# Optimization experiments

Measured on AMD Instinct MI355X. Metric: run time of the kernel, lower is better.

## Reference

```python
import jax, jax.numpy as jnp
import numpy as np

UNITS = 32
BACKBONE = 64

def lecun_tanh(x):
    return 1.7159 * jnp.tanh(0.666 * x)

def setup_inputs() -> dict:
    key = jax.random.key(0)
    ks = jax.random.split(key, 6)
    B, C, T, H, W = 4, 16, 32, 64, 64
    scale_b = 1.0 / np.sqrt(C + UNITS)
    scale_h = 1.0 / np.sqrt(BACKBONE)
    return {
        "x": jax.random.normal(ks[0], (B, C, T, H, W), jnp.float32),
        "Wb": jax.random.normal(ks[1], (BACKBONE, C + UNITS), jnp.float32) * scale_b,
        "bb": jnp.zeros((BACKBONE,), jnp.float32),
        "Wff1": jax.random.normal(ks[2], (UNITS, BACKBONE), jnp.float32) * scale_h,
        "bff1": jnp.zeros((UNITS,), jnp.float32),
        "Wff2": jax.random.normal(ks[3], (UNITS, BACKBONE), jnp.float32) * scale_h,
        "bff2": jnp.zeros((UNITS,), jnp.float32),
        "Wta": jax.random.normal(ks[4], (UNITS, BACKBONE), jnp.float32) * scale_h,
        "bta": jnp.zeros((UNITS,), jnp.float32),
        "Wtb": jax.random.normal(ks[5], (UNITS, BACKBONE), jnp.float32) * scale_h,
        "btb": jnp.zeros((UNITS,), jnp.float32),
    }

def reference(x, Wb, bb, Wff1, bff1, Wff2, bff2, Wta, bta, Wtb, btb):
    # x: (B, C, T, H, W) -> time-major (T, B, C, H, W) for the scan
    xs = jnp.transpose(x, (2, 0, 1, 3, 4))
    B, C, H, W = x.shape[0], x.shape[1], x.shape[3], x.shape[4]
    h0 = jnp.zeros((B, UNITS, H, W), x.dtype)
    ts = jnp.asarray(1.0, x.dtype)  # no timespans provided -> ts = 1.0

    def head(z, Wh, bh):  # channel-wise (1x1) linear: (B,K,H,W) -> (B,U,H,W)
        return jnp.einsum('bkhw,uk->buhw', z, Wh) + bh[None, :, None, None]

    def step(h, xt):
        z = jnp.concatenate([xt, h], axis=1)  # (B, C+U, H, W)
        z = lecun_tanh(jnp.einsum('bchw,kc->bkhw', z, Wb) + bb[None, :, None, None])
        ff1 = jnp.tanh(head(z, Wff1, bff1))
        ff2 = jnp.tanh(head(z, Wff2, bff2))
        t_a = head(z, Wta, bta)
        t_b = head(z, Wtb, btb)
        t_interp = jax.nn.sigmoid(t_a * ts + t_b)
        h_new = ff1 * (1.0 - t_interp) + t_interp * ff2
        return h_new, h_new

    _, ys = jax.lax.scan(step, h0, xs)  # ys: (T, B, U, H, W)
    # stack along dim=1 (batch_first) then permute(0,2,1,3,4) -> (B, U, T, H, W)
    return jnp.transpose(ys, (1, 2, 0, 3, 4))
```

## Files before the change

kernel.cpp:

```cpp
#include <hip/hip_runtime.h>
#include <hip/hip_bf16.h>


#define CIN      16
#define UNITS    32
#define BACKBONE 64
#define CZ       48
#define TSTEPS   32
#define HW       4096
#define NPIX     16
#define NTHREADS 256

typedef __attribute__((ext_vector_type(8))) short  short8;
typedef __attribute__((ext_vector_type(8))) __bf16 bf16x8;
typedef __attribute__((ext_vector_type(4))) float  float4v;
typedef __attribute__((ext_vector_type(4))) unsigned int uint4v;

#define BAR_LDS() asm volatile("s_waitcnt lgkmcnt(0)\n\ts_barrier" ::: "memory")

__device__ __forceinline__ unsigned short bf16_rne(float f) {
    unsigned u = __float_as_uint(f);
    return (unsigned short)((u + 0x7FFFu + ((u >> 16) & 1u)) >> 16);
}
__device__ __forceinline__ float bf16_tof(unsigned short h) {
    return __uint_as_float(((unsigned)h) << 16);
}
__device__ __forceinline__ unsigned cvt_pk_bf16(float lo, float hi) {
    unsigned r;
    asm("v_cvt_pk_bf16_f32 %0, %1, %2" : "=v"(r) : "v"(lo), "v"(hi));
    return r;
}

#if __has_builtin(__builtin_amdgcn_exp2f)
#define EXP2F(x) __builtin_amdgcn_exp2f(x)
#else
#define EXP2F(x) __expf(0.69314718056f * (x))
#endif
#if __has_builtin(__builtin_amdgcn_rcpf)
#define RCPF(x) __builtin_amdgcn_rcpf(x)
#else
#define RCPF(x) __fdividef(1.0f, (x))
#endif

__device__ __forceinline__ float lecun_tanh_f(float v) {
    float e = EXP2F(1.92166925f * v);
    return fmaf(-3.4318f, RCPF(e + 1.0f), 1.7159f);
}
__device__ __forceinline__ float tanh_f(float v) {
    float e = EXP2F(2.88539008f * v);
    return fmaf(-2.0f, RCPF(e + 1.0f), 1.0f);
}
__device__ __forceinline__ float sigmoid_f(float v) {
    float e = EXP2F(-1.44269504f * v);
    return RCPF(1.0f + e);
}
__device__ __forceinline__ float4v mfma16(bf16x8 a, bf16x8 b, float4v c) {
    return __builtin_amdgcn_mfma_f32_16x16x32_bf16(a, b, c, 0, 0, 0);
}
__device__ __forceinline__ void split8(const float* v, bf16x8& hi, bf16x8& lo) {
    short8 sh, sl;
    #pragma unroll
    for (int j = 0; j < 8; ++j) {
        unsigned short h = bf16_rne(v[j]);
        sh[j] = (short)h;
        sl[j] = (short)bf16_rne(v[j] - bf16_tof(h));
    }
    hi = __builtin_bit_cast(bf16x8, sh);
    lo = __builtin_bit_cast(bf16x8, sl);
}

__global__ __launch_bounds__(NTHREADS, 4)
void cfc_mfma_kernel(const float* __restrict__ x,   const float* __restrict__ Wb,
                     const float* __restrict__ bb,
                     const float* __restrict__ Wff1, const float* __restrict__ bff1,
                     const float* __restrict__ Wff2, const float* __restrict__ bff2,
                     const float* __restrict__ Wta,  const float* __restrict__ bta,
                     const float* __restrict__ Wtb,  const float* __restrict__ btb,
                     float* __restrict__ out)
{
    __shared__ unsigned hbuf[4][64];
    __shared__ unsigned abuf[8][64];

    const int tid  = threadIdx.x;
    const int w    = tid >> 6;
    const int lane = tid & 63;
    const int ln   = lane & 15;
    const int lq   = lane >> 4;

    const int gpix = blockIdx.x * NPIX;
    const int b    = gpix >> 12;
    const int pinb = gpix & 4095;
    const int mt   = w;

    bf16x8 Whhi, Whlo;
    {
        float v[8];
        #pragma unroll
        for (int j = 0; j < 8; ++j)
            v[j] = Wb[(mt * 16 + ln) * CZ + CIN + lq * 8 + j];
        split8(v, Whhi, Whlo);
    }
    bf16x8 Wxhi, Wxlo;
    {
        float v[8];
        #pragma unroll
        for (int j = 0; j < 8; ++j)
            v[j] = (lq < 2) ? Wb[(mt * 16 + ln) * CZ + lq * 8 + j] : 0.0f;
        split8(v, Wxhi, Wxlo);
    }
    float bbias[4];
    #pragma unroll
    for (int r = 0; r < 4; ++r) bbias[r] = bb[mt * 16 + lq * 4 + r];

    const int head = ln & 3;
    const float* Whp = (head == 0) ? Wff1 : (head == 1) ? Wff2 : (head == 2) ? Wta : Wtb;
    const int urow = (ln >> 2) * 8;
    bf16x8 Ah_hi[2][2], Ah_lo[2][2];
    #pragma unroll
    for (int i2 = 0; i2 < 2; ++i2) {
        #pragma unroll
        for (int kt = 0; kt < 2; ++kt) {
            float v[8];
            #pragma unroll
            for (int j = 0; j < 8; ++j) {
                int n = 32 * kt + (j >> 2) * 16 + lq * 4 + (j & 3);
                v[j] = Whp[(urow + 2 * w + i2) * BACKBONE + n];
            }
            split8(v, Ah_hi[i2][kt], Ah_lo[i2][kt]);
        }
    }
    const int ub = lq * 8;
    float hbias[2][4];
    #pragma unroll
    for (int i2 = 0; i2 < 2; ++i2) {
        int u2 = ub + 2 * w + i2;
        hbias[i2][0] = bff1[u2]; hbias[i2][1] = bff2[u2];
        hbias[i2][2] = bta[u2];  hbias[i2][3] = btb[u2];
    }

    unsigned xo[8];
    #pragma unroll
    for (int j = 0; j < 8; ++j) {
        int ch = (lq < 2) ? (lq * 8 + j) : 0;
        xo[j] = ((unsigned)(b * CIN + ch) * TSTEPS) * HW + (unsigned)(pinb + ln);
    }
    unsigned oo[2];
    #pragma unroll
    for (int i2 = 0; i2 < 2; ++i2)
        oo[i2] = ((unsigned)(b * UNITS + ub + 2 * w + i2) * TSTEPS) * HW
                 + (unsigned)(pinb + ln);

    auto packx = [&](const float (&v)[8]) {
        uint4v u = {cvt_pk_bf16(v[0], v[1]), cvt_pk_bf16(v[2], v[3]),
                    cvt_pk_bf16(v[4], v[5]), cvt_pk_bf16(v[6], v[7])};
        return __builtin_bit_cast(bf16x8, u);
    };

    ((unsigned*)hbuf)[tid] = 0u;
    float xv0[8] = {0,0,0,0,0,0,0,0}, xv1[8] = {0,0,0,0,0,0,0,0};
    if (lq < 2) {
        #pragma unroll
        for (int j = 0; j < 8; ++j) xv0[j] = x[xo[j]];
    }
    float4v xzA, xzB;
    {
        bf16x8 X0 = packx(xv0);
        float4v a = {bbias[0], bbias[1], bbias[2], bbias[3]};
        a = mfma16(Wxhi, X0, a);
        a = mfma16(Wxlo, X0, a);
        xzA = a;
    }
    if (lq < 2) {
        #pragma unroll
        for (int j = 0; j < 8; ++j) xv1[j] = x[xo[j] + HW];
    }
    __syncthreads();
    unsigned toff = 0;

    auto step = [&](int t, float4v xzc, float4v& xzn,
                    float (&xvi)[8], float (&xvp)[8]) {
        const int tl = (t + 2 < TSTEPS) ? t + 2 : TSTEPS - 1;
        if (lq < 2) {
            #pragma unroll
            for (int j = 0; j < 8; ++j) xvi[j] = x[xo[j] + (unsigned)tl * HW];
        }

        unsigned h0 = hbuf[0][lane], h1 = hbuf[1][lane];
        unsigned h2 = hbuf[2][lane], h3 = hbuf[3][lane];
        uint4v zv = {h0, h1, h2, h3};
        bf16x8 Z = __builtin_bit_cast(bf16x8, zv);
        float4v a = xzc;
        a = mfma16(Whhi, Z, a);
        a = mfma16(Whlo, Z, a);
        float g0 = lecun_tanh_f(a[0]);
        float g1 = lecun_tanh_f(a[1]);
        float g2 = lecun_tanh_f(a[2]);
        float g3 = lecun_tanh_f(a[3]);
        abuf[mt * 2 + 0][lane] = cvt_pk_bf16(g0, g1);
        abuf[mt * 2 + 1][lane] = cvt_pk_bf16(g2, g3);
        BAR_LDS();

        {
            bf16x8 X = packx(xvp);
            float4v q = {bbias[0], bbias[1], bbias[2], bbias[3]};
            q = mfma16(Wxhi, X, q);
            q = mfma16(Wxlo, X, q);
            xzn = q;
        }

        unsigned f0[4], f1[4];
        #pragma unroll
        for (int d = 0; d < 4; ++d) f0[d] = abuf[d][lane];
        #pragma unroll
        for (int d = 0; d < 4; ++d) f1[d] = abuf[4 + d][lane];
        uint4v w0 = {f0[0], f0[1], f0[2], f0[3]};
        uint4v w1 = {f1[0], f1[1], f1[2], f1[3]};
        bf16x8 A20 = __builtin_bit_cast(bf16x8, w0);
        bf16x8 A21 = __builtin_bit_cast(bf16x8, w1);

        float hn[2];
        #pragma unroll
        for (int i2 = 0; i2 < 2; ++i2) {
            float4v c = {hbias[i2][0], hbias[i2][1], hbias[i2][2], hbias[i2][3]};
            c = mfma16(Ah_hi[i2][0], A20, c);
            c = mfma16(Ah_lo[i2][0], A20, c);
            c = mfma16(Ah_hi[i2][1], A21, c);
            c = mfma16(Ah_lo[i2][1], A21, c);
            float f1g = tanh_f(c[0]);
            float f2g = tanh_f(c[1]);
            float ti  = sigmoid_f(c[2] + c[3]);
            float h   = fmaf(ti, f2g - f1g, f1g);
            out[oo[i2] + toff] = h;
            hn[i2] = h;
        }
        hbuf[w][lane] = cvt_pk_bf16(hn[0], hn[1]);
        BAR_LDS();
        toff += (unsigned)HW;
    };

    #pragma unroll 1
    for (int t = 0; t < TSTEPS; t += 2) {
        step(t,     xzA, xzB, xv0, xv1);
        step(t + 1, xzB, xzA, xv1, xv0);
    }
}

extern "C" void kernel_launch(void* const* d_in, const int* in_sizes, int n_in,
                              void* d_out, int out_size, void* d_ws, size_t ws_size,
                              hipStream_t stream) {
    dim3 grid(4 * HW / NPIX);
    cfc_mfma_kernel<<<grid, NTHREADS, 0, stream>>>(
        (const float*)d_in[0], (const float*)d_in[1], (const float*)d_in[2],
        (const float*)d_in[3], (const float*)d_in[4], (const float*)d_in[5],
        (const float*)d_in[6], (const float*)d_in[7], (const float*)d_in[8],
        (const float*)d_in[9], (const float*)d_in[10],
        (float*)d_out);
}
```

Measured before the change: 168.0 us.

## Process four pixel groups per block to amortize barriers and weight setup

Each block now handles 64 pixels as four independent 16-pixel groups, interleaving their recurrent steps between the same two barriers per timestep. This amortizes the per-block weight loading and splitting plus the barrier latency across more work, and gives the scheduler independent MFMA chains to overlap. In exchange the grid shrinks fourfold to 256 blocks, occupancy hints drop to one block per SIMD group, and register pressure rises from four sets of prefetched inputs, which may limit latency hiding.

```diff
diff --git a/kernel.cpp b/kernel.cpp
--- a/kernel.cpp
+++ b/kernel.cpp
@@ -8,7 +8,8 @@
 #define CZ       48
 #define TSTEPS   32
 #define HW       4096
-#define NPIX     16
+#define NG       4
+#define NPIX     64
 #define NTHREADS 256
 
 typedef __attribute__((ext_vector_type(8))) short  short8;
@@ -69,7 +70,7 @@
     lo = __builtin_bit_cast(bf16x8, sl);
 }
 
-__global__ __launch_bounds__(NTHREADS, 4)
+__global__ __launch_bounds__(NTHREADS, 1)
 void cfc_mfma_kernel(const float* __restrict__ x,   const float* __restrict__ Wb,
                      const float* __restrict__ bb,
                      const float* __restrict__ Wff1, const float* __restrict__ bff1,
@@ -78,8 +79,8 @@
                      const float* __restrict__ Wtb,  const float* __restrict__ btb,
                      float* __restrict__ out)
 {
-    __shared__ unsigned hbuf[4][64];
-    __shared__ unsigned abuf[8][64];
+    __shared__ unsigned hbuf[NG][4][64];
+    __shared__ unsigned abuf[NG][8][64];
 
     const int tid  = threadIdx.x;
     const int w    = tid >> 6;
@@ -156,92 +157,114 @@
         return __builtin_bit_cast(bf16x8, u);
     };
 
-    ((unsigned*)hbuf)[tid] = 0u;
-    float xv0[8] = {0,0,0,0,0,0,0,0}, xv1[8] = {0,0,0,0,0,0,0,0};
-    if (lq < 2) {
-        #pragma unroll
-        for (int j = 0; j < 8; ++j) xv0[j] = x[xo[j]];
-    }
-    float4v xzA, xzB;
-    {
-        bf16x8 X0 = packx(xv0);
+    #pragma unroll
+    for (int i = 0; i < NG; ++i)
+        ((unsigned*)hbuf)[tid + i * NTHREADS] = 0u;
+
+    float xva[NG][8], xvb[NG][8];
+    float4v xzA[NG], xzB[NG];
+    #pragma unroll
+    for (int g = 0; g < NG; ++g) {
+        #pragma unroll
+        for (int j = 0; j < 8; ++j) { xva[g][j] = 0.0f; xvb[g][j] = 0.0f; }
+        if (lq < 2) {
+            #pragma unroll
+            for (int j = 0; j < 8; ++j) xva[g][j] = x[xo[j] + g * 16];
+        }
+    }
+    #pragma unroll
+    for (int g = 0; g < NG; ++g) {
+        bf16x8 X0 = packx(xva[g]);
         float4v a = {bbias[0], bbias[1], bbias[2], bbias[3]};
         a = mfma16(Wxhi, X0, a);
         a = mfma16(Wxlo, X0, a);
-        xzA = a;
-    }
-    if (lq < 2) {
-        #pragma unroll
-        for (int j = 0; j < 8; ++j) xv1[j] = x[xo[j] + HW];
+        xzA[g] = a;
+    }
+    #pragma unroll
+    for (int g = 0; g < NG; ++g) {
+        if (lq < 2) {
+            #pragma unroll
+            for (int j = 0; j < 8; ++j) xvb[g][j] = x[xo[j] + g * 16 + HW];
+        }
     }
     __syncthreads();
     unsigned toff = 0;
 
-    auto step = [&](int t, float4v xzc, float4v& xzn,
-                    float (&xvi)[8], float (&xvp)[8]) {
+    auto step = [&](int t, float4v (&xzc)[NG], float4v (&xzn)[NG],
+                    float (&xvi)[NG][8], float (&xvp)[NG][8]) {
         const int tl = (t + 2 < TSTEPS) ? t + 2 : TSTEPS - 1;
         if (lq < 2) {
             #pragma unroll
-            for (int j = 0; j < 8; ++j) xvi[j] = x[xo[j] + (unsigned)tl * HW];
-        }
-
-        unsigned h0 = hbuf[0][lane], h1 = hbuf[1][lane];
-        unsigned h2 = hbuf[2][lane], h3 = hbuf[3][lane];
-        uint4v zv = {h0, h1, h2, h3};
-        bf16x8 Z = __builtin_bit_cast(bf16x8, zv);
-        float4v a = xzc;
-        a = mfma16(Whhi, Z, a);
-        a = mfma16(Whlo, Z, a);
-        float g0 = lecun_tanh_f(a[0]);
-        float g1 = lecun_tanh_f(a[1]);
-        float g2 = lecun_tanh_f(a[2]);
-        float g3 = lecun_tanh_f(a[3]);
-        abuf[mt * 2 + 0][lane] = cvt_pk_bf16(g0, g1);
-        abuf[mt * 2 + 1][lane] = cvt_pk_bf16(g2, g3);
+            for (int g = 0; g < NG; ++g)
+                #pragma unroll
+                for (int j = 0; j < 8; ++j)
+                    xvi[g][j] = x[xo[j] + g * 16 + (unsigned)tl * HW];
+        }
+
+        #pragma unroll
+        for (int g = 0; g < NG; ++g) {
+            unsigned h0 = hbuf[g][0][lane], h1 = hbuf[g][1][lane];
+            unsigned h2 = hbuf[g][2][lane], h3 = hbuf[g][3][lane];
+            uint4v zv = {h0, h1, h2, h3};
+            bf16x8 Z = __builtin_bit_cast(bf16x8, zv);
+            float4v a = xzc[g];
+            a = mfma16(Whhi, Z, a);
+            a = mfma16(Whlo, Z, a);
+            float g0 = lecun_tanh_f(a[0]);
+            float g1 = lecun_tanh_f(a[1]);
+            float g2 = lecun_tanh_f(a[2]);
+            float g3 = lecun_tanh_f(a[3]);
+            abuf[g][mt * 2 + 0][lane] = cvt_pk_bf16(g0, g1);
+            abuf[g][mt * 2 + 1][lane] = cvt_pk_bf16(g2, g3);
+        }
         BAR_LDS();
 
-        {
-            bf16x8 X = packx(xvp);
+        #pragma unroll
+        for (int g = 0; g < NG; ++g) {
+            bf16x8 X = packx(xvp[g]);
             float4v q = {bbias[0], bbias[1], bbias[2], bbias[3]};
             q = mfma16(Wxhi, X, q);
             q = mfma16(Wxlo, X, q);
-            xzn = q;
-        }
-
-        unsigned f0[4], f1[4];
-        #pragma unroll
-        for (int d = 0; d < 4; ++d) f0[d] = abuf[d][lane];
-        #pragma unroll
-        for (int d = 0; d < 4; ++d) f1[d] = abuf[4 + d][lane];
-        uint4v w0 = {f0[0], f0[1], f0[2], f0[3]};
-        uint4v w1 = {f1[0], f1[1], f1[2], f1[3]};
-        bf16x8 A20 = __builtin_bit_cast(bf16x8, w0);
-        bf16x8 A21 = __builtin_bit_cast(bf16x8, w1);
-
-        float hn[2];
-        #pragma unroll
-        for (int i2 = 0; i2 < 2; ++i2) {
-            float4v c = {hbias[i2][0], hbias[i2][1], hbias[i2][2], hbias[i2][3]};
-            c = mfma16(Ah_hi[i2][0], A20, c);
-            c = mfma16(Ah_lo[i2][0], A20, c);
-            c = mfma16(Ah_hi[i2][1], A21, c);
-            c = mfma16(Ah_lo[i2][1], A21, c);
-            float f1g = tanh_f(c[0]);
-            float f2g = tanh_f(c[1]);
-            float ti  = sigmoid_f(c[2] + c[3]);
-            float h   = fmaf(ti, f2g - f1g, f1g);
-            out[oo[i2] + toff] = h;
-            hn[i2] = h;
-        }
-        hbuf[w][lane] = cvt_pk_bf16(hn[0], hn[1]);
+            xzn[g] = q;
+        }
+
+        #pragma unroll
+        for (int g = 0; g < NG; ++g) {
+            unsigned f0[4], f1[4];
+            #pragma unroll
+            for (int d = 0; d < 4; ++d) f0[d] = abuf[g][d][lane];
+            #pragma unroll
+            for (int d = 0; d < 4; ++d) f1[d] = abuf[g][4 + d][lane];
+            uint4v w0 = {f0[0], f0[1], f0[2], f0[3]};
+            uint4v w1 = {f1[0], f1[1], f1[2], f1[3]};
+            bf16x8 A20 = __builtin_bit_cast(bf16x8, w0);
+            bf16x8 A21 = __builtin_bit_cast(bf16x8, w1);
+
+            float hn[2];
+            #pragma unroll
+            for (int i2 = 0; i2 < 2; ++i2) {
+                float4v c = {hbias[i2][0], hbias[i2][1], hbias[i2][2], hbias[i2][3]};
+                c = mfma16(Ah_hi[i2][0], A20, c);
+                c = mfma16(Ah_lo[i2][0], A20, c);
+                c = mfma16(Ah_hi[i2][1], A21, c);
+                c = mfma16(Ah_lo[i2][1], A21, c);
+                float f1g = tanh_f(c[0]);
+                float f2g = tanh_f(c[1]);
+                float ti  = sigmoid_f(c[2] + c[3]);
+                float h   = fmaf(ti, f2g - f1g, f1g);
+                out[oo[i2] + g * 16 + toff] = h;
+                hn[i2] = h;
+            }
+            hbuf[g][w][lane] = cvt_pk_bf16(hn[0], hn[1]);
+        }
         BAR_LDS();
         toff += (unsigned)HW;
     };
 
     #pragma unroll 1
     for (int t = 0; t < TSTEPS; t += 2) {
-        step(t,     xzA, xzB, xv0, xv1);
-        step(t + 1, xzB, xzA, xv1, xv0);
+        step(t,     xzA, xzB, xva, xvb);
+        step(t + 1, xzB, xzA, xvb, xva);
     }
 }
 
```

Result: faster. 158.5 us (-5.7%).

## Distribute x loads across all waves and share via LDS staging buffer

Applied to the files above, without the earlier changes.

Previously every wave redundantly loaded all 16 input channels per pixel (8 loads per lane in half the lanes). Now each wave loads only two channels, packs them to bf16 and writes them to a small shared xbuf, and all waves read the full fragment back from LDS. The prefetch distance is extended by one step to cover the extra staging hop. This removes four-fold redundant global loads at the cost of extra LDS traffic and relies on existing barriers for ordering.

```diff
diff --git a/kernel.cpp b/kernel.cpp
--- a/kernel.cpp
+++ b/kernel.cpp
@@ -80,6 +80,7 @@
 {
     __shared__ unsigned hbuf[4][64];
     __shared__ unsigned abuf[8][64];
+    __shared__ unsigned xbuf[8][16];
 
     const int tid  = threadIdx.x;
     const int w    = tid >> 6;
@@ -138,52 +139,60 @@
         hbias[i2][2] = bta[u2];  hbias[i2][3] = btb[u2];
     }
 
-    unsigned xo[8];
-    #pragma unroll
-    for (int j = 0; j < 8; ++j) {
-        int ch = (lq < 2) ? (lq * 8 + j) : 0;
-        xo[j] = ((unsigned)(b * CIN + ch) * TSTEPS) * HW + (unsigned)(pinb + ln);
-    }
+    const int  xr  = 2 * w + (lq & 1);
+    const bool xpr = (lq < 2);
+    const unsigned xi0 = ((unsigned)(b * CIN + 2 * xr) * TSTEPS) * HW
+                         + (unsigned)(pinb + ln);
+    const unsigned xi1 = xi0 + (unsigned)(TSTEPS * HW);
+
+    const int xrow = (lq & 1) * 4;
+
     unsigned oo[2];
     #pragma unroll
     for (int i2 = 0; i2 < 2; ++i2)
         oo[i2] = ((unsigned)(b * UNITS + ub + 2 * w + i2) * TSTEPS) * HW
                  + (unsigned)(pinb + ln);
 
-    auto packx = [&](const float (&v)[8]) {
-        uint4v u = {cvt_pk_bf16(v[0], v[1]), cvt_pk_bf16(v[2], v[3]),
-                    cvt_pk_bf16(v[4], v[5]), cvt_pk_bf16(v[6], v[7])};
+    auto xfrag = [&](const unsigned (&xf)[4]) {
+        uint4v u = {xf[0], xf[1], xf[2], xf[3]};
         return __builtin_bit_cast(bf16x8, u);
     };
 
     ((unsigned*)hbuf)[tid] = 0u;
-    float xv0[8] = {0,0,0,0,0,0,0,0}, xv1[8] = {0,0,0,0,0,0,0,0};
-    if (lq < 2) {
-        #pragma unroll
-        for (int j = 0; j < 8; ++j) xv0[j] = x[xo[j]];
-    }
+    if (xpr) {
+        float a0 = x[xi0], a1 = x[xi1];
+        xbuf[xr][ln] = cvt_pk_bf16(a0, a1);
+    }
+    __syncthreads();
     float4v xzA, xzB;
     {
-        bf16x8 X0 = packx(xv0);
+        unsigned xf[4];
+        #pragma unroll
+        for (int jj = 0; jj < 4; ++jj) xf[jj] = xbuf[xrow + jj][ln];
+        bf16x8 X0 = xfrag(xf);
         float4v a = {bbias[0], bbias[1], bbias[2], bbias[3]};
         a = mfma16(Wxhi, X0, a);
         a = mfma16(Wxlo, X0, a);
         xzA = a;
     }
-    if (lq < 2) {
-        #pragma unroll
-        for (int j = 0; j < 8; ++j) xv1[j] = x[xo[j] + HW];
+    __syncthreads();
+    float pc0 = 0.f, pc1 = 0.f, pn0 = 0.f, pn1 = 0.f;
+    if (xpr) {
+        float a0 = x[xi0 + HW], a1 = x[xi1 + HW];
+        xbuf[xr][ln] = cvt_pk_bf16(a0, a1);
+        pc0 = x[xi0 + 2u * HW]; pc1 = x[xi1 + 2u * HW];
     }
     __syncthreads();
     unsigned toff = 0;
 
     auto step = [&](int t, float4v xzc, float4v& xzn,
-                    float (&xvi)[8], float (&xvp)[8]) {
-        const int tl = (t + 2 < TSTEPS) ? t + 2 : TSTEPS - 1;
-        if (lq < 2) {
-            #pragma unroll
-            for (int j = 0; j < 8; ++j) xvi[j] = x[xo[j] + (unsigned)tl * HW];
-        }
+                    float& c0, float& c1, float& n0, float& n1) {
+        const unsigned tl = (unsigned)((t + 3 < TSTEPS) ? t + 3 : TSTEPS - 1);
+        if (xpr) { n0 = x[xi0 + tl * HW]; n1 = x[xi1 + tl * HW]; }
+
+        unsigned xf[4];
+        #pragma unroll
+        for (int jj = 0; jj < 4; ++jj) xf[jj] = xbuf[xrow + jj][ln];
 
         unsigned h0 = hbuf[0][lane], h1 = hbuf[1][lane];
         unsigned h2 = hbuf[2][lane], h3 = hbuf[3][lane];
@@ -200,8 +209,9 @@
         abuf[mt * 2 + 1][lane] = cvt_pk_bf16(g2, g3);
         BAR_LDS();
 
+        if (xpr) xbuf[xr][ln] = cvt_pk_bf16(c0, c1);
         {
-            bf16x8 X = packx(xvp);
+            bf16x8 X = xfrag(xf);
             float4v q = {bbias[0], bbias[1], bbias[2], bbias[3]};
             q = mfma16(Wxhi, X, q);
             q = mfma16(Wxlo, X, q);
@@ -240,8 +250,8 @@
 
     #pragma unroll 1
     for (int t = 0; t < TSTEPS; t += 2) {
-        step(t,     xzA, xzB, xv0, xv1);
-        step(t + 1, xzB, xzA, xv1, xv0);
+        step(t,     xzA, xzB, pc0, pc1, pn0, pn1);
+        step(t + 1, xzB, xzA, pn0, pn1, pc0, pc1);
     }
 }
 
```

Measured after the change: 150.9 us. -10.2%, faster.
